# Kernel optimization log

Hardware: AMD Instinct MI355X
Metric: run time of the kernel (lower is better)

The kernel has to match this reference:

```python
import jax, jax.numpy as jnp
import numpy as np

B, N, C, P, HEADS = 4, 1024, 128, 4, 16
D = P * P * C          # 2048 token feature dim
DH = D // HEADS        # 128 per-head dim
MASK_NUM = 25
SCALE = 64 ** (-0.5)   # hardcoded in the original module


def setup_inputs() -> dict:
    key = jax.random.key(0)
    ks = jax.random.split(key, 12)
    s = 0.05
    return {
        "x": jax.random.normal(ks[0], (B, N, D), jnp.float32),
        "Wq": jax.random.normal(ks[1], (C, C), jnp.float32) * s,
        "bq": jax.random.normal(ks[2], (C,), jnp.float32) * s,
        "Wk": jax.random.normal(ks[3], (C, C), jnp.float32) * s,
        "bk": jax.random.normal(ks[4], (C,), jnp.float32) * s,
        "Wv": jax.random.normal(ks[5], (C, C), jnp.float32) * s,
        "bv": jax.random.normal(ks[6], (C,), jnp.float32) * s,
        "Wl": jax.random.normal(ks[7], (1, C), jnp.float32) * s,
        "bl": jax.random.normal(ks[8], (1,), jnp.float32) * s,
        "Wo": jax.random.normal(ks[9], (D, D), jnp.float32) * (1.0 / np.sqrt(D)),
        "bo": jax.random.normal(ks[10], (D,), jnp.float32) * s,
        "stage": 0,
    }


def reference(x, Wq, bq, Wk, bk, Wv, bv, Wl, bl, Wo, bo, stage):
    b, n, d = x.shape
    # 1x1 conv over the channel axis is a per-position linear map; the
    # token<->image rearranges are layout-only, so apply it directly on
    # (b, n, p*p, C).
    xr = x.reshape(b, n, P * P, C)
    q = jnp.einsum('bnpc,oc->bnpo', xr, Wq) + bq   # conv_q (1x1)
    k = jnp.einsum('bnpc,oc->bnpo', xr, Wk) + bk   # conv_k (1x1)
    v = jnp.einsum('bnpc,oc->bnpo', xr, Wv) + bv   # conv_v (1x1)

    # Token-importance mask: avg over the p*p positions (AdaptiveAvgPool2d
    # (1, C)), linear C->1, softmax over tokens.
    m = q.mean(axis=2)                              # (b, n, C)
    logits = (m @ Wl.T + bl)[..., 0]                # (b, n)
    mask = jax.nn.softmax(logits, axis=-1)
    # threshold = mask_num-th smallest value per row; values strictly above
    # it are snapped to 1, the rest keep their (tiny) softmax value.
    thr = -jax.lax.top_k(-mask, MASK_NUM)[0][..., -1:]   # (b, 1)... per-row
    mask = jnp.where(mask > thr, jnp.float32(1.0), mask)  # (b, n)

    kf = k.reshape(b, n, d) * mask[:, :, None]
    vf = v.reshape(b, n, d) * mask[:, :, None]

    qh = q.reshape(b, n, HEADS, DH).transpose(0, 2, 1, 3)   # (b, h, n, dh)
    kh = kf.reshape(b, n, HEADS, DH).transpose(0, 2, 1, 3)
    vh = vf.reshape(b, n, HEADS, DH).transpose(0, 2, 1, 3)

    dots = jnp.einsum('bhid,bhjd->bhij', qh, kh) * SCALE
    attn = jax.nn.softmax(dots, axis=-1)
    out = jnp.einsum('bhij,bhjd->bhid', attn, vh)
    out = out.transpose(0, 2, 1, 3).reshape(b, n, d)
    return out @ Wo.T + bo                          # to_out (dropout p=0)
```

## Files before the change

### kernel.cpp

```cpp
#include <hip/hip_runtime.h>
#include <stdint.h>

typedef __attribute__((ext_vector_type(8))) short s8v;
typedef __attribute__((ext_vector_type(4))) short s4v;
typedef __attribute__((ext_vector_type(4))) float f4v;

#define MFMA(a,b,c) __builtin_amdgcn_mfma_f32_16x16x32_bf16((a),(b),(c),0,0,0)

__device__ __forceinline__ short f2bf(float f){
  union { float f; unsigned u; } a; a.f = f;
  unsigned r = (a.u + 0x7fffu + ((a.u >> 16) & 1u)) >> 16;
  return (short)r;
}

__device__ __forceinline__ void gld16(const void* g, void* l){
  __builtin_amdgcn_global_load_lds((const __attribute__((address_space(1))) void*)g,
                                   (__attribute__((address_space(3))) void*)l, 16, 0, 0);
}

__global__ void k_wcomb(const float* __restrict__ Wq, const float* __restrict__ bq,
                        const float* __restrict__ Wl, const float* __restrict__ bl,
                        float* __restrict__ wcomb){
  int c = threadIdx.x;
  float s = 0.f;
  for (int o = 0; o < 128; ++o) s += Wl[o] * Wq[o*128 + c];
  wcomb[c] = s;
  if (c == 0){
    float t = 0.f; for (int o = 0; o < 128; ++o) t += Wl[o] * bq[o];
    wcomb[128] = t + bl[0];
  }
}

__global__ void k_conv_w(const float* __restrict__ Wq, const float* __restrict__ Wk,
                         const float* __restrict__ Wv, const float* __restrict__ Wo,
                         short* __restrict__ wq16, short* __restrict__ wk16,
                         short* __restrict__ wv16, short* __restrict__ wo16){
  int i = blockIdx.x*256 + threadIdx.x;
  wo16[i] = f2bf(Wo[i]);
  if (i < 16384){ wq16[i] = f2bf(Wq[i]); wk16[i] = f2bf(Wk[i]); wv16[i] = f2bf(Wv[i]); }
}

__global__ __launch_bounds__(256) void k_conv_x(const float* __restrict__ x, const float* __restrict__ wcomb,
                                                short* __restrict__ x16, float* __restrict__ logits){
  __shared__ float wc[128];
  __shared__ float part[4];
  int t = blockIdx.x, tid = threadIdx.x;
  if (tid < 128) wc[tid] = wcomb[tid];
  __syncthreads();
  const float* xp = x + (size_t)t*2048;
  short* op = x16 + (size_t)t*2048;
  float s = 0.f;
  #pragma unroll
  for (int j = 0; j < 2; ++j){
    int idx = j*1024 + tid*4;
    float4 v = *(const float4*)(xp + idx);
    s4v o; o.x = f2bf(v.x); o.y = f2bf(v.y); o.z = f2bf(v.z); o.w = f2bf(v.w);
    *(s4v*)(op + idx) = o;
    s += v.x*wc[idx&127] + v.y*wc[(idx+1)&127] + v.z*wc[(idx+2)&127] + v.w*wc[(idx+3)&127];
  }
  for (int off = 32; off; off >>= 1) s += __shfl_down(s, off);
  if ((tid&63) == 0) part[tid>>6] = s;
  __syncthreads();
  if (tid == 0) logits[t] = (part[0]+part[1]+part[2]+part[3])*(1.f/16.f) + wcomb[128];
}

__global__ __launch_bounds__(64) void k_mask(const float* __restrict__ logits, float* __restrict__ maskout){
  int b = blockIdx.x, lane = threadIdx.x;
  float v[16];
  #pragma unroll
  for (int i = 0; i < 16; ++i) v[i] = logits[b*1024 + i*64 + lane];
  float mx = v[0];
  #pragma unroll
  for (int i = 1; i < 16; ++i) mx = fmaxf(mx, v[i]);
  #pragma unroll
  for (int off = 32; off; off >>= 1) mx = fmaxf(mx, __shfl_xor(mx, off));
  float s = 0.f;
  #pragma unroll
  for (int i = 0; i < 16; ++i){ v[i] = __expf(v[i] - mx); s += v[i]; }
  #pragma unroll
  for (int off = 32; off; off >>= 1) s += __shfl_xor(s, off);
  float p[16];
  #pragma unroll
  for (int i = 0; i < 16; ++i){ p[i] = v[i] / s; v[i] = p[i]; }
  float thr = 0.f;
  for (int k = 0; k < 25; ++k){
    float lm = v[0]; int li = 0;
    #pragma unroll
    for (int i = 1; i < 16; ++i){ if (v[i] < lm){ lm = v[i]; li = i; } }
    float gm = lm;
    #pragma unroll
    for (int off = 32; off; off >>= 1) gm = fminf(gm, __shfl_xor(gm, off));
    if (k == 24) thr = gm;
    unsigned long long ball = __ballot(lm == gm);
    int owner = __ffsll((unsigned long long)ball) - 1;
    bool rm = (lane == owner);
    #pragma unroll
    for (int i = 0; i < 16; ++i){ if (rm && i == li) v[i] = 2.0f; }
  }
  #pragma unroll
  for (int i = 0; i < 16; ++i)
    maskout[b*1024 + i*64 + lane] = p[i] > thr ? 1.0f : p[i];
}

__global__ __launch_bounds__(256) void k_qkv3(const short* __restrict__ x16,
                                              const short* __restrict__ wq16, const short* __restrict__ wk16,
                                              const short* __restrict__ wv16,
                                              const float* __restrict__ bq, const float* __restrict__ bk,
                                              const float* __restrict__ bv,
                                              short* __restrict__ q16, short* __restrict__ k16,
                                              short* __restrict__ v16o){
  __shared__ short At[64*136];
  __shared__ short Wt[128*136];
  int tid = threadIdx.x, lane = tid&63, w = tid>>6;
  int m0 = blockIdx.x*64;
  #pragma unroll
  for (int i = 0; i < 4; ++i){
    int ch = tid + 256*i; int r = ch>>4, c8 = (ch&15)*8;
    *(s8v*)&At[r*136 + c8] = *(const s8v*)(x16 + (size_t)(m0+r)*128 + c8);
  }
  int ln = lane&15, q = lane>>4;
  const short* ws[3] = {wq16, wk16, wv16};
  const float* bs[3] = {bq, bk, bv};
  short*       os[3] = {q16, k16, v16o};
  for (int ps = 0; ps < 3; ++ps){
    if (ps) __syncthreads();
    #pragma unroll
    for (int i = 0; i < 8; ++i){
      int ch = tid + 256*i; int r = ch>>4, c8 = (ch&15)*8;
      *(s8v*)&Wt[r*136 + c8] = *(const s8v*)(ws[ps] + r*128 + c8);
    }
    __syncthreads();
    f4v acc[8];
    #pragma unroll
    for (int cb = 0; cb < 8; ++cb) acc[cb] = f4v{0.f,0.f,0.f,0.f};
    #pragma unroll
    for (int ks = 0; ks < 4; ++ks){
      s8v a = *(const s8v*)&At[(w*16+ln)*136 + ks*32 + q*8];
      #pragma unroll
      for (int cb = 0; cb < 8; ++cb){
        s8v bb = *(const s8v*)&Wt[(cb*16+ln)*136 + ks*32 + q*8];
        acc[cb] = MFMA(a, bb, acc[cb]);
      }
    }
    float sc = (ps == 0) ? 0.125f : 1.0f;
    short* op = os[ps];
    const float* bp = bs[ps];
    #pragma unroll
    for (int cb = 0; cb < 8; ++cb){
      int col = cb*16 + ln;
      float bv2 = bp[col];
      #pragma unroll
      for (int r = 0; r < 4; ++r){
        int row = m0 + w*16 + q*4 + r;
        op[(size_t)row*128 + col] = f2bf((acc[cb][r] + bv2)*sc);
      }
    }
  }
}

__global__ __launch_bounds__(256) void k_vtrans(const short* __restrict__ v16, short* __restrict__ vt16){
  __shared__ short T[128*136];
  int bh = blockIdx.x, nt = blockIdx.y;
  int b = bh>>4, h = bh&15, n0 = nt*128;
  int tid = threadIdx.x;
  #pragma unroll
  for (int i = 0; i < 8; ++i){
    int ch = tid + 256*i; int r = ch>>4, c8 = (ch&15)*8;
    *(s8v*)&T[r*136 + c8] = *(const s8v*)(v16 + (size_t)(b*1024 + n0 + r)*2048 + h*128 + c8);
  }
  __syncthreads();
  #pragma unroll
  for (int i = 0; i < 8; ++i){
    int ch = tid + 256*i; int c = ch>>4, r8 = (ch&15)*8;
    s8v o;
    #pragma unroll
    for (int j = 0; j < 8; ++j) o[j] = T[(r8+j)*136 + c];
    *(s8v*)(vt16 + (size_t)(bh*128 + c)*1024 + n0 + r8) = o;
  }
}

__global__ __launch_bounds__(256, 2) void k_attn(const short* __restrict__ q16, const short* __restrict__ k16,
                                                 const short* __restrict__ vt16, const float* __restrict__ maskp,
                                                 short* __restrict__ a16){
  __shared__ short Ks[64*128];
  __shared__ short Vs[128*64];
  __shared__ short Ps[128*72];
  int it = blockIdx.x, h = blockIdx.y, b = blockIdx.z;
  int i0 = it*128;
  int tid = threadIdx.x, lane = tid&63, w = tid>>6;
  int ln = lane&15, q = lane>>4;
  s8v aq[2][4];
  const short* qbase = q16 + (size_t)(b*1024 + i0 + w*32)*2048 + h*128;
  #pragma unroll
  for (int rb = 0; rb < 2; ++rb)
    #pragma unroll
    for (int ks = 0; ks < 4; ++ks)
      aq[rb][ks] = *(const s8v*)(qbase + (size_t)(rb*16+ln)*2048 + ks*32 + q*8);
  f4v o[2][8];
  #pragma unroll
  for (int rb = 0; rb < 2; ++rb)
    #pragma unroll
    for (int cb = 0; cb < 8; ++cb) o[rb][cb] = f4v{0.f,0.f,0.f,0.f};
  float mo[2][4], lo[2][4];
  #pragma unroll
  for (int rb = 0; rb < 2; ++rb)
    #pragma unroll
    for (int r = 0; r < 4; ++r){ mo[rb][r] = -3.0e38f; lo[rb][r] = 0.f; }
  const short* kbase = k16 + (size_t)(b*1024)*2048 + h*128;
  const short* vbase = vt16 + (size_t)((b*16+h)*128)*1024;
  for (int jt = 0; jt < 16; ++jt){
    int j0 = jt*64;
    __syncthreads();
    #pragma unroll
    for (int t = 0; t < 4; ++t){
      int r = w*16 + t*4 + (lane>>4);
      int c = lane&15;
      gld16(kbase + (size_t)(j0 + r)*2048 + ((c ^ (r&7))*8), &Ks[(w*16 + t*4)*128]);
    }
    #pragma unroll
    for (int t = 0; t < 4; ++t){
      int r = w*32 + t*8 + (lane>>3);
      int c = lane&7;
      gld16(vbase + (size_t)r*1024 + j0 + ((c ^ (r&7))*8), &Vs[(w*32 + t*8)*64]);
    }
    __syncthreads();
    f4v sa[2][4];
    #pragma unroll
    for (int rb = 0; rb < 2; ++rb)
      #pragma unroll
      for (int cb = 0; cb < 4; ++cb) sa[rb][cb] = f4v{0.f,0.f,0.f,0.f};
    #pragma unroll
    for (int ks = 0; ks < 4; ++ks)
      #pragma unroll
      for (int cb = 0; cb < 4; ++cb){
        int r = cb*16 + ln;
        s8v bb = *(const s8v*)&Ks[r*128 + (((ks*4 + q) ^ (ln&7))*8)];
        sa[0][cb] = MFMA(aq[0][ks], bb, sa[0][cb]);
        sa[1][cb] = MFMA(aq[1][ks], bb, sa[1][cb]);
      }
    float mv[4];
    #pragma unroll
    for (int cb = 0; cb < 4; ++cb) mv[cb] = maskp[b*1024 + j0 + cb*16 + ln];
    #pragma unroll
    for (int rb = 0; rb < 2; ++rb){
      float sv[4][4];
      #pragma unroll
      for (int cb = 0; cb < 4; ++cb)
        #pragma unroll
        for (int r = 0; r < 4; ++r) sv[cb][r] = sa[rb][cb][r]*mv[cb];
      float mx[4];
      #pragma unroll
      for (int r = 0; r < 4; ++r) mx[r] = fmaxf(fmaxf(sv[0][r], sv[1][r]), fmaxf(sv[2][r], sv[3][r]));
      #pragma unroll
      for (int off = 1; off < 16; off <<= 1)
        #pragma unroll
        for (int r = 0; r < 4; ++r) mx[r] = fmaxf(mx[r], __shfl_xor(mx[r], off));
      float mnew[4], al[4], rs[4];
      #pragma unroll
      for (int r = 0; r < 4; ++r){
        mnew[r] = fmaxf(mo[rb][r], mx[r]);
        al[r] = __expf(mo[rb][r] - mnew[r]);
        rs[r] = 0.f;
      }
      #pragma unroll
      for (int cb = 0; cb < 4; ++cb)
        #pragma unroll
        for (int r = 0; r < 4; ++r){
          float pp = __expf(sv[cb][r] - mnew[r]);
          rs[r] += pp;
          Ps[(w*32 + rb*16 + q*4 + r)*72 + cb*16 + ln] = f2bf(pp*mv[cb]);
        }
      #pragma unroll
      for (int off = 1; off < 16; off <<= 1)
        #pragma unroll
        for (int r = 0; r < 4; ++r) rs[r] += __shfl_xor(rs[r], off);
      #pragma unroll
      for (int r = 0; r < 4; ++r){ lo[rb][r] = lo[rb][r]*al[r] + rs[r]; mo[rb][r] = mnew[r]; }
      #pragma unroll
      for (int cb = 0; cb < 8; ++cb)
        #pragma unroll
        for (int r = 0; r < 4; ++r) o[rb][cb][r] *= al[r];
    }
    __syncthreads();
    #pragma unroll
    for (int ks = 0; ks < 2; ++ks){
      s8v pa[2];
      #pragma unroll
      for (int rb = 0; rb < 2; ++rb) pa[rb] = *(const s8v*)&Ps[(w*32 + rb*16 + ln)*72 + ks*32 + q*8];
      #pragma unroll
      for (int cb = 0; cb < 8; ++cb){
        int r = cb*16 + ln;
        s8v bb = *(const s8v*)&Vs[r*64 + (((ks*4 + q) ^ (ln&7))*8)];
        o[0][cb] = MFMA(pa[0], bb, o[0][cb]);
        o[1][cb] = MFMA(pa[1], bb, o[1][cb]);
      }
    }
  }
  #pragma unroll
  for (int rb = 0; rb < 2; ++rb)
    #pragma unroll
    for (int cb = 0; cb < 8; ++cb){
      int col = cb*16 + ln;
      #pragma unroll
      for (int r = 0; r < 4; ++r){
        int row = i0 + w*32 + rb*16 + q*4 + r;
        a16[(size_t)(b*1024 + row)*2048 + h*128 + col] = f2bf(o[rb][cb][r] / lo[rb][r]);
      }
    }
}

__global__ __launch_bounds__(256) void k_out(const short* __restrict__ a16, const short* __restrict__ wo16,
                                             const float* __restrict__ bo, float* __restrict__ out){
  __shared__ short As[128*64];
  __shared__ short Bs[128*64];
  int tid = threadIdx.x, lane = tid&63, w = tid>>6;
  int m0 = blockIdx.x*128, n0 = blockIdx.y*128;
  int wrow = (w>>1)*64, wcol = (w&1)*64;
  int ln = lane&15, q = lane>>4;
  f4v acc[4][4];
  #pragma unroll
  for (int i = 0; i < 4; ++i)
    #pragma unroll
    for (int j = 0; j < 4; ++j) acc[i][j] = f4v{0.f,0.f,0.f,0.f};
  for (int it = 0; it < 32; ++it){
    int k0 = it*64;
    __syncthreads();
    #pragma unroll
    for (int t = 0; t < 4; ++t){
      int r = w*32 + t*8 + (lane>>3);
      int c = lane&7;
      int gc8 = (c ^ (r&7))*8;
      gld16(a16  + (size_t)(m0+r)*2048 + k0 + gc8, &As[(w*32 + t*8)*64]);
      gld16(wo16 + (size_t)(n0+r)*2048 + k0 + gc8, &Bs[(w*32 + t*8)*64]);
    }
    __syncthreads();
    #pragma unroll
    for (int ks = 0; ks < 2; ++ks){
      s8v a[4], bb[4];
      int swz = ((ks*4 + q) ^ (ln&7))*8;
      #pragma unroll
      for (int i = 0; i < 4; ++i){
        a[i]  = *(const s8v*)&As[(wrow + i*16 + ln)*64 + swz];
        bb[i] = *(const s8v*)&Bs[(wcol + i*16 + ln)*64 + swz];
      }
      #pragma unroll
      for (int i = 0; i < 4; ++i)
        #pragma unroll
        for (int j = 0; j < 4; ++j) acc[i][j] = MFMA(a[i], bb[j], acc[i][j]);
    }
  }
  #pragma unroll
  for (int j = 0; j < 4; ++j){
    int col = n0 + wcol + j*16 + ln;
    float bv = bo[col];
    #pragma unroll
    for (int i = 0; i < 4; ++i)
      #pragma unroll
      for (int r = 0; r < 4; ++r){
        int row = m0 + wrow + i*16 + q*4 + r;
        out[(size_t)row*2048 + col] = acc[i][j][r] + bv;
      }
  }
}

extern "C" void kernel_launch(void* const* d_in, const int* in_sizes, int n_in,
                              void* d_out, int out_size, void* d_ws, size_t ws_size,
                              hipStream_t stream){
  const float* x  = (const float*)d_in[0];
  const float* Wq = (const float*)d_in[1];
  const float* bq = (const float*)d_in[2];
  const float* Wk = (const float*)d_in[3];
  const float* bk = (const float*)d_in[4];
  const float* Wv = (const float*)d_in[5];
  const float* bv = (const float*)d_in[6];
  const float* Wl = (const float*)d_in[7];
  const float* bl = (const float*)d_in[8];
  const float* Wo = (const float*)d_in[9];
  const float* bo = (const float*)d_in[10];
  float* out = (float*)d_out;

  char* p = (char*)d_ws;
  size_t off = 0;
  auto take = [&](size_t bytes)->char*{ char* r = p + off; off = (off + bytes + 255) & ~(size_t)255; return r; };
  short* x16   = (short*)take(16777216);
  short* q16   = (short*)take(16777216);
  short* k16   = (short*)take(16777216);
  short* v16   = (short*)take(16777216);
  short* vt16  = (short*)take(16777216);
  short* wo16  = (short*)take(8388608);
  short* wq16  = (short*)take(32768);
  short* wk16  = (short*)take(32768);
  short* wv16  = (short*)take(32768);
  float* wcomb = (float*)take(4*129);
  float* logits= (float*)take(4*4096);
  float* maskp = (float*)take(4*4096);
  short* a16 = x16;

  k_wcomb <<<1, 128, 0, stream>>>(Wq, bq, Wl, bl, wcomb);
  k_conv_w<<<16384, 256, 0, stream>>>(Wq, Wk, Wv, Wo, wq16, wk16, wv16, wo16);
  k_conv_x<<<4096, 256, 0, stream>>>(x, wcomb, x16, logits);
  k_mask  <<<4, 64, 0, stream>>>(logits, maskp);
  k_qkv3  <<<1024, 256, 0, stream>>>(x16, wq16, wk16, wv16, bq, bk, bv, q16, k16, v16);
  k_vtrans<<<dim3(64, 8), 256, 0, stream>>>(v16, vt16);
  k_attn  <<<dim3(8, 16, 4), 256, 0, stream>>>(q16, k16, vt16, maskp, a16);
  k_out   <<<dim3(32, 16), 256, 0, stream>>>(a16, wo16, bo, out);
}
```

Before: 298.8 us.

## Fuse V transpose and mask scaling into QKV, use exp2 and MFMA row sums

The QKV projection now writes V directly in transposed layout through LDS and premultiplies K and V by the token mask, which removes the separate transpose kernel and the per-tile mask loads in attention. Q is prescaled by scale*log2e, so attention can use exp2f. Attention computes S^T with swapped MFMA operands so each lane owns a full row for a cheaper max reduction, gets row sums from an extra MFMA against a ones vector, and drops one barrier. The weight-prep kernels are merged into one launch. Precision changes slightly because the mask and the row sums now pass through bf16.

```diff
diff --git a/kernel.cpp b/kernel.cpp
--- a/kernel.cpp
+++ b/kernel.cpp
@@ -12,32 +12,35 @@
   unsigned r = (a.u + 0x7fffu + ((a.u >> 16) & 1u)) >> 16;
   return (short)r;
 }
+__device__ __forceinline__ unsigned pk2(float a, float b){
+  return (unsigned)(unsigned short)f2bf(a) | ((unsigned)(unsigned short)f2bf(b) << 16);
+}
 
 __device__ __forceinline__ void gld16(const void* g, void* l){
   __builtin_amdgcn_global_load_lds((const __attribute__((address_space(1))) void*)g,
                                    (__attribute__((address_space(3))) void*)l, 16, 0, 0);
 }
 
-__global__ void k_wcomb(const float* __restrict__ Wq, const float* __restrict__ bq,
-                        const float* __restrict__ Wl, const float* __restrict__ bl,
-                        float* __restrict__ wcomb){
-  int c = threadIdx.x;
-  float s = 0.f;
-  for (int o = 0; o < 128; ++o) s += Wl[o] * Wq[o*128 + c];
-  wcomb[c] = s;
-  if (c == 0){
-    float t = 0.f; for (int o = 0; o < 128; ++o) t += Wl[o] * bq[o];
-    wcomb[128] = t + bl[0];
-  }
-}
-
-__global__ void k_conv_w(const float* __restrict__ Wq, const float* __restrict__ Wk,
-                         const float* __restrict__ Wv, const float* __restrict__ Wo,
-                         short* __restrict__ wq16, short* __restrict__ wk16,
-                         short* __restrict__ wv16, short* __restrict__ wo16){
+__global__ void k_prep(const float* __restrict__ Wq, const float* __restrict__ Wk,
+                       const float* __restrict__ Wv, const float* __restrict__ Wo,
+                       const float* __restrict__ bq, const float* __restrict__ Wl,
+                       const float* __restrict__ bl,
+                       short* __restrict__ wq16, short* __restrict__ wk16,
+                       short* __restrict__ wv16, short* __restrict__ wo16,
+                       float* __restrict__ wcomb){
   int i = blockIdx.x*256 + threadIdx.x;
   wo16[i] = f2bf(Wo[i]);
   if (i < 16384){ wq16[i] = f2bf(Wq[i]); wk16[i] = f2bf(Wk[i]); wv16[i] = f2bf(Wv[i]); }
+  if (blockIdx.x == 0 && threadIdx.x < 128){
+    int c = threadIdx.x;
+    float s = 0.f;
+    for (int o = 0; o < 128; ++o) s += Wl[o] * Wq[o*128 + c];
+    wcomb[c] = s;
+    if (c == 0){
+      float t = 0.f; for (int o = 0; o < 128; ++o) t += Wl[o] * bq[o];
+      wcomb[128] = t + bl[0];
+    }
+  }
 }
 
 __global__ __launch_bounds__(256) void k_conv_x(const float* __restrict__ x, const float* __restrict__ wcomb,
@@ -106,22 +109,24 @@
                                               const short* __restrict__ wq16, const short* __restrict__ wk16,
                                               const short* __restrict__ wv16,
                                               const float* __restrict__ bq, const float* __restrict__ bk,
-                                              const float* __restrict__ bv,
+                                              const float* __restrict__ bv, const float* __restrict__ maskp,
                                               short* __restrict__ q16, short* __restrict__ k16,
-                                              short* __restrict__ v16o){
+                                              short* __restrict__ vt16){
   __shared__ short At[64*136];
   __shared__ short Wt[128*136];
   int tid = threadIdx.x, lane = tid&63, w = tid>>6;
-  int m0 = blockIdx.x*64;
+  int n0 = blockIdx.x*64, p = blockIdx.y, b = blockIdx.z;
   #pragma unroll
   for (int i = 0; i < 4; ++i){
     int ch = tid + 256*i; int r = ch>>4, c8 = (ch&15)*8;
-    *(s8v*)&At[r*136 + c8] = *(const s8v*)(x16 + (size_t)(m0+r)*128 + c8);
+    *(s8v*)&At[r*136 + c8] = *(const s8v*)(x16 + (size_t)(b*1024 + n0 + r)*2048 + p*128 + c8);
   }
   int ln = lane&15, q = lane>>4;
+  float mvr[4];
+  #pragma unroll
+  for (int r = 0; r < 4; ++r) mvr[r] = maskp[b*1024 + n0 + w*16 + q*4 + r];
   const short* ws[3] = {wq16, wk16, wv16};
   const float* bs[3] = {bq, bk, bv};
-  short*       os[3] = {q16, k16, v16o};
   for (int ps = 0; ps < 3; ++ps){
     if (ps) __syncthreads();
     #pragma unroll
@@ -142,49 +147,50 @@
         acc[cb] = MFMA(a, bb, acc[cb]);
       }
     }
-    float sc = (ps == 0) ? 0.125f : 1.0f;
-    short* op = os[ps];
     const float* bp = bs[ps];
-    #pragma unroll
-    for (int cb = 0; cb < 8; ++cb){
-      int col = cb*16 + ln;
-      float bv2 = bp[col];
-      #pragma unroll
-      for (int r = 0; r < 4; ++r){
-        int row = m0 + w*16 + q*4 + r;
-        op[(size_t)row*128 + col] = f2bf((acc[cb][r] + bv2)*sc);
-      }
-    }
-  }
-}
-
-__global__ __launch_bounds__(256) void k_vtrans(const short* __restrict__ v16, short* __restrict__ vt16){
-  __shared__ short T[128*136];
-  int bh = blockIdx.x, nt = blockIdx.y;
-  int b = bh>>4, h = bh&15, n0 = nt*128;
-  int tid = threadIdx.x;
-  #pragma unroll
-  for (int i = 0; i < 8; ++i){
-    int ch = tid + 256*i; int r = ch>>4, c8 = (ch&15)*8;
-    *(s8v*)&T[r*136 + c8] = *(const s8v*)(v16 + (size_t)(b*1024 + n0 + r)*2048 + h*128 + c8);
-  }
-  __syncthreads();
-  #pragma unroll
-  for (int i = 0; i < 8; ++i){
-    int ch = tid + 256*i; int c = ch>>4, r8 = (ch&15)*8;
-    s8v o;
-    #pragma unroll
-    for (int j = 0; j < 8; ++j) o[j] = T[(r8+j)*136 + c];
-    *(s8v*)(vt16 + (size_t)(bh*128 + c)*1024 + n0 + r8) = o;
+    if (ps < 2){
+      float sc = (ps == 0) ? 0.180336881f : 1.0f;
+      short* op = (ps == 0) ? q16 : k16;
+      #pragma unroll
+      for (int cb = 0; cb < 8; ++cb){
+        int col = cb*16 + ln;
+        float bv2 = bp[col];
+        #pragma unroll
+        for (int r = 0; r < 4; ++r){
+          int n = n0 + w*16 + q*4 + r;
+          float mm = (ps == 1) ? mvr[r] : 1.0f;
+          op[(size_t)(b*1024 + n)*2048 + p*128 + col] = f2bf((acc[cb][r] + bv2)*sc*mm);
+        }
+      }
+    } else {
+      __syncthreads();
+      #pragma unroll
+      for (int cb = 0; cb < 8; ++cb){
+        int col = cb*16 + ln;
+        float bv2 = bp[col];
+        #pragma unroll
+        for (int r = 0; r < 4; ++r)
+          At[(w*16 + q*4 + r)*136 + col] = f2bf((acc[cb][r] + bv2)*mvr[r]);
+      }
+      __syncthreads();
+      #pragma unroll
+      for (int i = 0; i < 4; ++i){
+        int ch = tid + 256*i; int c = ch>>3, n8 = (ch&7)*8;
+        s8v o;
+        #pragma unroll
+        for (int j = 0; j < 8; ++j) o[j] = At[(n8+j)*136 + c];
+        *(s8v*)(vt16 + (size_t)((b*16+p)*128 + c)*1024 + n0 + n8) = o;
+      }
+    }
   }
 }
 
 __global__ __launch_bounds__(256, 2) void k_attn(const short* __restrict__ q16, const short* __restrict__ k16,
-                                                 const short* __restrict__ vt16, const float* __restrict__ maskp,
-                                                 short* __restrict__ a16){
+                                                 const short* __restrict__ vt16, short* __restrict__ a16){
   __shared__ short Ks[64*128];
   __shared__ short Vs[128*64];
   __shared__ short Ps[128*72];
+  __shared__ float alS[128];
   int it = blockIdx.x, h = blockIdx.y, b = blockIdx.z;
   int i0 = it*128;
   int tid = threadIdx.x, lane = tid&63, w = tid>>6;
@@ -192,20 +198,21 @@
   s8v aq[2][4];
   const short* qbase = q16 + (size_t)(b*1024 + i0 + w*32)*2048 + h*128;
   #pragma unroll
-  for (int rb = 0; rb < 2; ++rb)
+  for (int g = 0; g < 2; ++g)
     #pragma unroll
     for (int ks = 0; ks < 4; ++ks)
-      aq[rb][ks] = *(const s8v*)(qbase + (size_t)(rb*16+ln)*2048 + ks*32 + q*8);
-  f4v o[2][8];
-  #pragma unroll
-  for (int rb = 0; rb < 2; ++rb)
-    #pragma unroll
-    for (int cb = 0; cb < 8; ++cb) o[rb][cb] = f4v{0.f,0.f,0.f,0.f};
-  float mo[2][4], lo[2][4];
-  #pragma unroll
-  for (int rb = 0; rb < 2; ++rb)
-    #pragma unroll
-    for (int r = 0; r < 4; ++r){ mo[rb][r] = -3.0e38f; lo[rb][r] = 0.f; }
+      aq[g][ks] = *(const s8v*)(qbase + (size_t)(g*16+ln)*2048 + ks*32 + q*8);
+  s8v ones;
+  #pragma unroll
+  for (int j = 0; j < 8; ++j) ones[j] = (short)0x3F80;
+  f4v o[2][8], o9[2];
+  #pragma unroll
+  for (int g = 0; g < 2; ++g){
+    #pragma unroll
+    for (int cb = 0; cb < 8; ++cb) o[g][cb] = f4v{0.f,0.f,0.f,0.f};
+    o9[g] = f4v{0.f,0.f,0.f,0.f};
+  }
+  float mo[2] = {-3.0e38f, -3.0e38f};
   const short* kbase = k16 + (size_t)(b*1024)*2048 + h*128;
   const short* vbase = vt16 + (size_t)((b*16+h)*128)*1024;
   for (int jt = 0; jt < 16; ++jt){
@@ -224,87 +231,79 @@
       gld16(vbase + (size_t)r*1024 + j0 + ((c ^ (r&7))*8), &Vs[(w*32 + t*8)*64]);
     }
     __syncthreads();
-    f4v sa[2][4];
-    #pragma unroll
-    for (int rb = 0; rb < 2; ++rb)
-      #pragma unroll
-      for (int cb = 0; cb < 4; ++cb) sa[rb][cb] = f4v{0.f,0.f,0.f,0.f};
+    f4v st[2][4];
+    #pragma unroll
+    for (int g = 0; g < 2; ++g)
+      #pragma unroll
+      for (int mb = 0; mb < 4; ++mb) st[g][mb] = f4v{0.f,0.f,0.f,0.f};
     #pragma unroll
     for (int ks = 0; ks < 4; ++ks)
       #pragma unroll
-      for (int cb = 0; cb < 4; ++cb){
-        int r = cb*16 + ln;
-        s8v bb = *(const s8v*)&Ks[r*128 + (((ks*4 + q) ^ (ln&7))*8)];
-        sa[0][cb] = MFMA(aq[0][ks], bb, sa[0][cb]);
-        sa[1][cb] = MFMA(aq[1][ks], bb, sa[1][cb]);
-      }
-    float mv[4];
-    #pragma unroll
-    for (int cb = 0; cb < 4; ++cb) mv[cb] = maskp[b*1024 + j0 + cb*16 + ln];
-    #pragma unroll
-    for (int rb = 0; rb < 2; ++rb){
-      float sv[4][4];
-      #pragma unroll
-      for (int cb = 0; cb < 4; ++cb)
-        #pragma unroll
-        for (int r = 0; r < 4; ++r) sv[cb][r] = sa[rb][cb][r]*mv[cb];
-      float mx[4];
-      #pragma unroll
-      for (int r = 0; r < 4; ++r) mx[r] = fmaxf(fmaxf(sv[0][r], sv[1][r]), fmaxf(sv[2][r], sv[3][r]));
-      #pragma unroll
-      for (int off = 1; off < 16; off <<= 1)
-        #pragma unroll
-        for (int r = 0; r < 4; ++r) mx[r] = fmaxf(mx[r], __shfl_xor(mx[r], off));
-      float mnew[4], al[4], rs[4];
-      #pragma unroll
-      for (int r = 0; r < 4; ++r){
-        mnew[r] = fmaxf(mo[rb][r], mx[r]);
-        al[r] = __expf(mo[rb][r] - mnew[r]);
-        rs[r] = 0.f;
-      }
-      #pragma unroll
-      for (int cb = 0; cb < 4; ++cb)
-        #pragma unroll
-        for (int r = 0; r < 4; ++r){
-          float pp = __expf(sv[cb][r] - mnew[r]);
-          rs[r] += pp;
-          Ps[(w*32 + rb*16 + q*4 + r)*72 + cb*16 + ln] = f2bf(pp*mv[cb]);
-        }
-      #pragma unroll
-      for (int off = 1; off < 16; off <<= 1)
-        #pragma unroll
-        for (int r = 0; r < 4; ++r) rs[r] += __shfl_xor(rs[r], off);
-      #pragma unroll
-      for (int r = 0; r < 4; ++r){ lo[rb][r] = lo[rb][r]*al[r] + rs[r]; mo[rb][r] = mnew[r]; }
+      for (int mb = 0; mb < 4; ++mb){
+        s8v ka = *(const s8v*)&Ks[(mb*16+ln)*128 + (((ks*4 + q) ^ (ln&7))*8)];
+        st[0][mb] = MFMA(ka, aq[0][ks], st[0][mb]);
+        st[1][mb] = MFMA(ka, aq[1][ks], st[1][mb]);
+      }
+    #pragma unroll
+    for (int g = 0; g < 2; ++g){
+      float mx = st[g][0][0];
+      #pragma unroll
+      for (int mb = 0; mb < 4; ++mb)
+        #pragma unroll
+        for (int r = 0; r < 4; ++r) mx = fmaxf(mx, st[g][mb][r]);
+      mx = fmaxf(mx, __shfl_xor(mx, 16));
+      mx = fmaxf(mx, __shfl_xor(mx, 32));
+      float mnew = fmaxf(mo[g], mx);
+      float al = exp2f(mo[g] - mnew);
+      mo[g] = mnew;
+      int prow = (w*32 + g*16 + ln)*72;
+      #pragma unroll
+      for (int mb = 0; mb < 4; ++mb){
+        uint2 u;
+        u.x = pk2(exp2f(st[g][mb][0] - mnew), exp2f(st[g][mb][1] - mnew));
+        u.y = pk2(exp2f(st[g][mb][2] - mnew), exp2f(st[g][mb][3] - mnew));
+        *(uint2*)&Ps[prow + mb*16 + q*4] = u;
+      }
+      if (q == 0) alS[w*32 + g*16 + ln] = al;
+    }
+    float alr[2][4];
+    #pragma unroll
+    for (int g = 0; g < 2; ++g)
+      #pragma unroll
+      for (int r = 0; r < 4; ++r) alr[g][r] = alS[w*32 + g*16 + q*4 + r];
+    #pragma unroll
+    for (int g = 0; g < 2; ++g){
       #pragma unroll
       for (int cb = 0; cb < 8; ++cb)
         #pragma unroll
-        for (int r = 0; r < 4; ++r) o[rb][cb][r] *= al[r];
-    }
-    __syncthreads();
+        for (int r = 0; r < 4; ++r) o[g][cb][r] *= alr[g][r];
+      #pragma unroll
+      for (int r = 0; r < 4; ++r) o9[g][r] *= alr[g][r];
+    }
     #pragma unroll
     for (int ks = 0; ks < 2; ++ks){
       s8v pa[2];
       #pragma unroll
-      for (int rb = 0; rb < 2; ++rb) pa[rb] = *(const s8v*)&Ps[(w*32 + rb*16 + ln)*72 + ks*32 + q*8];
+      for (int g = 0; g < 2; ++g) pa[g] = *(const s8v*)&Ps[(w*32 + g*16 + ln)*72 + ks*32 + q*8];
       #pragma unroll
       for (int cb = 0; cb < 8; ++cb){
-        int r = cb*16 + ln;
-        s8v bb = *(const s8v*)&Vs[r*64 + (((ks*4 + q) ^ (ln&7))*8)];
+        s8v bb = *(const s8v*)&Vs[(cb*16+ln)*64 + (((ks*4 + q) ^ (ln&7))*8)];
         o[0][cb] = MFMA(pa[0], bb, o[0][cb]);
         o[1][cb] = MFMA(pa[1], bb, o[1][cb]);
       }
-    }
-  }
-  #pragma unroll
-  for (int rb = 0; rb < 2; ++rb)
+      o9[0] = MFMA(pa[0], ones, o9[0]);
+      o9[1] = MFMA(pa[1], ones, o9[1]);
+    }
+  }
+  #pragma unroll
+  for (int g = 0; g < 2; ++g)
     #pragma unroll
     for (int cb = 0; cb < 8; ++cb){
       int col = cb*16 + ln;
       #pragma unroll
       for (int r = 0; r < 4; ++r){
-        int row = i0 + w*32 + rb*16 + q*4 + r;
-        a16[(size_t)(b*1024 + row)*2048 + h*128 + col] = f2bf(o[rb][cb][r] / lo[rb][r]);
+        int row = i0 + w*32 + g*16 + q*4 + r;
+        a16[(size_t)(b*1024 + row)*2048 + h*128 + col] = f2bf(o[g][cb][r] / o9[g][r]);
       }
     }
 }
@@ -385,7 +384,6 @@
   short* x16   = (short*)take(16777216);
   short* q16   = (short*)take(16777216);
   short* k16   = (short*)take(16777216);
-  short* v16   = (short*)take(16777216);
   short* vt16  = (short*)take(16777216);
   short* wo16  = (short*)take(8388608);
   short* wq16  = (short*)take(32768);
@@ -396,12 +394,10 @@
   float* maskp = (float*)take(4*4096);
   short* a16 = x16;
 
-  k_wcomb <<<1, 128, 0, stream>>>(Wq, bq, Wl, bl, wcomb);
-  k_conv_w<<<16384, 256, 0, stream>>>(Wq, Wk, Wv, Wo, wq16, wk16, wv16, wo16);
+  k_prep  <<<16384, 256, 0, stream>>>(Wq, Wk, Wv, Wo, bq, Wl, bl, wq16, wk16, wv16, wo16, wcomb);
   k_conv_x<<<4096, 256, 0, stream>>>(x, wcomb, x16, logits);
   k_mask  <<<4, 64, 0, stream>>>(logits, maskp);
-  k_qkv3  <<<1024, 256, 0, stream>>>(x16, wq16, wk16, wv16, bq, bk, bv, q16, k16, v16);
-  k_vtrans<<<dim3(64, 8), 256, 0, stream>>>(v16, vt16);
-  k_attn  <<<dim3(8, 16, 4), 256, 0, stream>>>(q16, k16, vt16, maskp, a16);
+  k_qkv3  <<<dim3(16, 16, 4), 256, 0, stream>>>(x16, wq16, wk16, wv16, bq, bk, bv, maskp, q16, k16, vt16);
+  k_attn  <<<dim3(8, 16, 4), 256, 0, stream>>>(q16, k16, vt16, a16);
   k_out   <<<dim3(32, 16), 256, 0, stream>>>(a16, wo16, bo, out);
 }
```

Result: faster. 262.1 us (-12.3%).
